# Kernel optimization log

Measured on AMD Instinct MI355X. Metric: run time of the kernel, lower is better.

The kernel has to match this reference:

```python
import jax, jax.numpy as jnp
import numpy as np

B, K, P, N, COEF_D = 32, 2, 256, 8192, 10  # batch, parts, kp-per-part, cloud points
BETA = 0.1
SEP_FACTOR = 8.0
W_CHF, W_COV, W_SURF, W_JOINT, W_REG, W_SEP = 1.0, 1.0, 5.0, 1.0, 0.01, 2.0
# separation-loss pair indices (static, same as torch buffers select1/select2)
SEL1 = np.tile(np.arange(P), P - 1)
SEL2 = np.concatenate([np.arange(j, j + P) % P for j in range(1, P)])


def _pdist(a, b):
    # a: (..., M, 3), b: (..., N, 3) -> (..., M, N) euclidean distances
    d2 = (jnp.sum(a * a, -1)[..., :, None] + jnp.sum(b * b, -1)[..., None, :]
          - 2.0 * jnp.einsum('...mc,...nc->...mn', a, b))
    return jnp.sqrt(jnp.maximum(d2, 1e-12))


def _smooth_l1(pred, target, beta=BETA):
    d = jnp.abs(pred - target)
    return jnp.where(d < beta, 0.5 * d * d / beta, d - 0.5 * beta)


def setup_inputs() -> dict:
    key = jax.random.key(0)
    ks = jax.random.split(key, 10)
    return {
        'coefs': jax.random.normal(ks[0], (B, K * P, COEF_D), jnp.float32),
        'part_pred_kps': jax.random.normal(ks[1], (B, K, P, 3), jnp.float32),
        'part_nodes': jax.random.normal(ks[2], (B, K, P, 3), jnp.float32),
        'cloud': jax.random.normal(ks[3], (B, N, 3), jnp.float32),
        'cloud_cls': jax.random.randint(ks[4], (B, N), 0, K, jnp.int64),
        'pred_joint_loc': jax.random.normal(ks[5], (B, K - 1, 3), jnp.float32),
        'pred_joint_axis': jax.random.normal(ks[6], (B, K - 1, 3), jnp.float32),
        'gt_joint_loc': jax.random.normal(ks[7], (B, K - 1, 3), jnp.float32),
        'gt_joint_axis': jax.random.normal(ks[8], (B, K - 1, 3), jnp.float32),
        'gt_part_scale': jax.random.uniform(ks[9], (B, K, 3), jnp.float32),
    }


def _forward(coefs, part_pred_kps, part_nodes, cloud,
             pred_joint_loc, pred_joint_axis, gt_joint_loc, gt_joint_axis,
             gt_part_scale, cloud_cls):
    # ---- part chamfer (brute) over all parts at once: (B,K,M,N) ----
    d_chf = _pdist(part_pred_kps, part_nodes)
    fwd = jnp.min(d_chf, axis=3).mean(axis=(0, 2))   # (K,)
    bwd = jnp.min(d_chf, axis=2).mean(axis=(0, 2))   # (K,)
    chf_loss = jnp.mean(fwd + bwd)

    # ---- coverage loss: masked per-part pc extremes vs node extremes ----
    mask = cloud_cls[:, None, :] == jnp.arange(K)[None, :, None]  # (B,K,N)
    big = jnp.float32(1e9)
    pc = cloud[:, None, :, :]                                      # (B,1,N,3)
    pc_max = jnp.max(jnp.where(mask[..., None], pc, -big), axis=2)  # (B,K,3)
    pc_min = jnp.min(jnp.where(mask[..., None], pc, big), axis=2)
    kp_max = jnp.max(part_nodes, axis=2)                            # (B,K,3)
    kp_min = jnp.min(part_nodes, axis=2)
    cov_loss = jnp.mean((_smooth_l1(kp_max, pc_max) + _smooth_l1(kp_min, pc_min)) * 0.5)

    # ---- separation loss ----
    a = part_nodes[:, :, SEL1, :]
    b = part_nodes[:, :, SEL2, :]
    dist_sep = jnp.linalg.norm(a - b, axis=-1)                      # (B,K,L)
    thr = (jnp.linalg.norm(gt_part_scale, axis=-1) / SEP_FACTOR)[:, :, None]
    sep_loss = jnp.mean(jnp.maximum(0.0, thr - dist_sep))

    # ---- surface loss: single-side chamfer nodes -> cloud ----
    nodes = part_nodes.reshape(B, K * P, 3)
    d_surf = _pdist(nodes, cloud)                                   # (B, K*P, N)
    surf_loss = jnp.min(d_surf, axis=2).mean()

    # ---- joint loss ----
    dot = jnp.sum(pred_joint_axis * gt_joint_axis, -1)
    na = jnp.linalg.norm(pred_joint_axis, axis=-1)
    nb = jnp.linalg.norm(gt_joint_axis, axis=-1)
    loss_axis = 1.0 - (dot / jnp.maximum(na * nb, 1e-8)).mean()
    ngt = gt_joint_axis / jnp.linalg.norm(gt_joint_axis, axis=-1, keepdims=True)
    p = gt_joint_loc
    q = gt_joint_loc + ngt
    r = pred_joint_loc
    x = p - q
    t = jnp.sum((r - q) * x, -1, keepdims=True) / jnp.sum(x * x, -1, keepdims=True)
    loss_loc = jnp.linalg.norm(t * (p - q) + (q - r), axis=-1).mean()
    joint_loss = loss_loc * 1.0 + loss_axis * 0.5  # revolute: loc_weight=1, axis_weight=0.5

    reg_loss = jnp.mean(coefs * coefs)

    return (chf_loss * W_CHF + cov_loss * W_COV + surf_loss * W_SURF
            + joint_loss * W_JOINT + reg_loss * W_REG + sep_loss * W_SEP)


def reference(coefs, part_pred_kps, part_nodes, cloud, cloud_cls,
              pred_joint_loc, pred_joint_axis, gt_joint_loc, gt_joint_axis,
              gt_part_scale):
    return _forward(coefs, part_pred_kps, part_nodes, cloud,
                    pred_joint_loc, pred_joint_axis, gt_joint_loc,
                    gt_joint_axis, gt_part_scale, cloud_cls)
```

## Files before the change

kernel.cpp:

```cpp
#include <hip/hip_runtime.h>
#include <math.h>

#define NB 32
#define KK 2
#define PP 256
#define NCLOUD 8192
#define NNODES 512
#define NCOEF 163840
#define SURF0 385
#define NCHUNK 16
#define NSURF (NB * NCHUNK)
#define NBLK (SURF0 + NSURF)

#define SL_SEP 0
#define SL_COV 256
#define SL_REG 320
#define SL_JNT 384
#define PCHF 512
#define PART0 131584

__device__ inline float waveSum(float v) {
#pragma unroll
  for (int o = 32; o > 0; o >>= 1) v += __shfl_down(v, o);
  return v;
}
__device__ inline float waveMax(float v) {
#pragma unroll
  for (int o = 32; o > 0; o >>= 1) v = fmaxf(v, __shfl_down(v, o));
  return v;
}
__device__ inline float waveMin(float v) {
#pragma unroll
  for (int o = 32; o > 0; o >>= 1) v = fminf(v, __shfl_down(v, o));
  return v;
}
__device__ inline float smooth_l1(float d) {
  d = fabsf(d);
  return d < 0.1f ? 5.0f * d * d : d - 0.05f;
}

__global__ __launch_bounds__(256) void mega_kernel(
    const float* __restrict__ coefs,
    const float* __restrict__ preds,
    const float* __restrict__ nodes,
    const float* __restrict__ cloud,
    const int* __restrict__ cls,
    const float* __restrict__ pjl, const float* __restrict__ pja,
    const float* __restrict__ gjl, const float* __restrict__ gja,
    const float* __restrict__ gps,
    float* __restrict__ ws, float* __restrict__ out) {
  const int bid = blockIdx.x;
  const int t = threadIdx.x;
  const int wave = t >> 6, lane = t & 63;
  __shared__ float4 sh4[512];
  __shared__ float shg[2048];
  __shared__ float red[12][4];

  if (bid < 256) {
    const int bk = bid >> 2;
    const int h = bid & 3;
    const float* pb = preds + (size_t)bk * PP * 3;
    const float* nbp = nodes + (size_t)bk * PP * 3;
    {
      float x = pb[3 * t], y = pb[3 * t + 1], z = pb[3 * t + 2];
      sh4[t] = make_float4(x, y, z, x * x + y * y + z * z);
      x = nbp[3 * t]; y = nbp[3 * t + 1]; z = nbp[3 * t + 2];
      sh4[256 + t] = make_float4(x, y, z, x * x + y * y + z * z);
    }
    __syncthreads();
    float4 ptv[4], ntv[4];
#pragma unroll
    for (int q = 0; q < 4; ++q) {
      ptv[q] = sh4[lane + q * 64];
      ntv[q] = sh4[256 + lane + q * 64];
    }
    const float s0 = gps[bk * 3 + 0], s1 = gps[bk * 3 + 1], s2 = gps[bk * 3 + 2];
    const float thr = sqrtf(s0 * s0 + s1 * s1 + s2 * s2) * 0.125f;
    float g1[4], g2[4], sep = 0.0f;
#pragma unroll
    for (int q = 0; q < 4; ++q) { g1[q] = 1e30f; g2[q] = 1e30f; }
    const int j0 = h * 64 + wave * 16;
#pragma unroll 4
    for (int jj = 0; jj < 16; ++jj) {
      const int j = j0 + jj;
      const float4 pj = sh4[j];
      const float4 nj = sh4[256 + j];
#pragma unroll
      for (int q = 0; q < 4; ++q) {
        float dot = fmaf(ptv[q].x, nj.x, fmaf(ptv[q].y, nj.y, ptv[q].z * nj.z));
        g1[q] = fminf(g1[q], fmaf(-2.0f, dot, nj.w));
        dot = fmaf(ntv[q].x, pj.x, fmaf(ntv[q].y, pj.y, ntv[q].z * pj.z));
        g2[q] = fminf(g2[q], fmaf(-2.0f, dot, pj.w));
        dot = fmaf(ntv[q].x, nj.x, fmaf(ntv[q].y, nj.y, ntv[q].z * nj.z));
        const float d2 = fmaf(-2.0f, dot, ntv[q].w + nj.w);
        const float d = sqrtf(fmaxf(d2, 0.0f));
        if (j != lane + q * 64) sep += fmaxf(thr - d, 0.0f);
      }
    }
#pragma unroll
    for (int q = 0; q < 4; ++q) {
      shg[wave * 256 + lane + q * 64] = ptv[q].w + g1[q];
      shg[1024 + wave * 256 + lane + q * 64] = ntv[q].w + g2[q];
    }
    __syncthreads();
    float* pc = ws + PCHF + (size_t)bid * 512;
    pc[t] = fminf(fminf(shg[t], shg[256 + t]),
                  fminf(shg[512 + t], shg[768 + t]));
    pc[256 + t] = fminf(fminf(shg[1024 + t], shg[1280 + t]),
                        fminf(shg[1536 + t], shg[1792 + t]));
    sep = waveSum(sep);
    if (lane == 0) red[0][wave] = sep;
    __syncthreads();
    if (t == 0)
      ws[SL_SEP + bid] = red[0][0] + red[0][1] + red[0][2] + red[0][3];

  } else if (bid < 320) {
    const int bk = bid - 256;
    const int b = bk >> 1;
    const int k = bk & 1;
    float pmax0 = -1e9f, pmax1 = -1e9f, pmax2 = -1e9f;
    float pmin0 = 1e9f, pmin1 = 1e9f, pmin2 = 1e9f;
    const float* cb = cloud + (size_t)b * NCLOUD * 3;
    const int* lb = cls + (size_t)b * NCLOUD;
    for (int i = t; i < NCLOUD; i += 256) {
      if (lb[i] == k) {
        const float x = cb[i * 3 + 0], y = cb[i * 3 + 1], z = cb[i * 3 + 2];
        pmax0 = fmaxf(pmax0, x); pmax1 = fmaxf(pmax1, y); pmax2 = fmaxf(pmax2, z);
        pmin0 = fminf(pmin0, x); pmin1 = fminf(pmin1, y); pmin2 = fminf(pmin2, z);
      }
    }
    const float* nb = nodes + (size_t)bk * PP * 3;
    const float kx = nb[t * 3 + 0], ky = nb[t * 3 + 1], kz = nb[t * 3 + 2];
    pmax0 = waveMax(pmax0); pmax1 = waveMax(pmax1); pmax2 = waveMax(pmax2);
    pmin0 = waveMin(pmin0); pmin1 = waveMin(pmin1); pmin2 = waveMin(pmin2);
    float kmax0 = waveMax(kx), kmax1 = waveMax(ky), kmax2 = waveMax(kz);
    float kmin0 = waveMin(kx), kmin1 = waveMin(ky), kmin2 = waveMin(kz);
    if (lane == 0) {
      red[0][wave] = pmax0; red[1][wave] = pmax1; red[2][wave] = pmax2;
      red[3][wave] = pmin0; red[4][wave] = pmin1; red[5][wave] = pmin2;
      red[6][wave] = kmax0; red[7][wave] = kmax1; red[8][wave] = kmax2;
      red[9][wave] = kmin0; red[10][wave] = kmin1; red[11][wave] = kmin2;
    }
    __syncthreads();
    if (t == 0) {
      float v[12];
#pragma unroll
      for (int q = 0; q < 12; ++q) {
        if (q < 3 || (q >= 6 && q < 9))
          v[q] = fmaxf(fmaxf(red[q][0], red[q][1]), fmaxf(red[q][2], red[q][3]));
        else
          v[q] = fminf(fminf(red[q][0], red[q][1]), fminf(red[q][2], red[q][3]));
      }
      float s = 0.0f;
#pragma unroll
      for (int c2 = 0; c2 < 3; ++c2)
        s += 0.5f * (smooth_l1(v[6 + c2] - v[0 + c2]) + smooth_l1(v[9 + c2] - v[3 + c2]));
      ws[SL_COV + bk] = s;
    }

  } else if (bid < 384) {
    const int r = bid - 320;
    const float4* c4 = (const float4*)coefs;
    float v = 0.0f;
    for (int i = r * 256 + t; i < NCOEF / 4; i += 64 * 256) {
      const float4 q = c4[i];
      v += q.x * q.x + q.y * q.y + q.z * q.z + q.w * q.w;
    }
    v = waveSum(v);
    if (lane == 0) red[0][wave] = v;
    __syncthreads();
    if (t == 0)
      ws[SL_REG + r] = red[0][0] + red[0][1] + red[0][2] + red[0][3];

  } else if (bid == 384) {
    float cosv = 0.0f, locv = 0.0f;
    if (t < NB) {
      const float axj = pja[t * 3 + 0], ayj = pja[t * 3 + 1], azj = pja[t * 3 + 2];
      const float gx = gja[t * 3 + 0], gy = gja[t * 3 + 1], gz = gja[t * 3 + 2];
      const float dot = axj * gx + ayj * gy + azj * gz;
      const float na = sqrtf(axj * axj + ayj * ayj + azj * azj);
      const float nbn = sqrtf(gx * gx + gy * gy + gz * gz);
      cosv = dot / fmaxf(na * nbn, 1e-8f);
      const float ux = gx / nbn, uy = gy / nbn, uz = gz / nbn;
      const float px = gjl[t * 3 + 0], py = gjl[t * 3 + 1], pz = gjl[t * 3 + 2];
      const float qx = px + ux, qy = py + uy, qz = pz + uz;
      const float rx = pjl[t * 3 + 0], ry = pjl[t * 3 + 1], rz = pjl[t * 3 + 2];
      const float xx = px - qx, xy = py - qy, xz = pz - qz;
      const float tnum = (rx - qx) * xx + (ry - qy) * xy + (rz - qz) * xz;
      const float tden = xx * xx + xy * xy + xz * xz;
      const float tv = tnum / tden;
      const float vx = tv * xx + (qx - rx);
      const float vy = tv * xy + (qy - ry);
      const float vz = tv * xz + (qz - rz);
      locv = sqrtf(vx * vx + vy * vy + vz * vz);
    }
    cosv = waveSum(cosv);
    locv = waveSum(locv);
    if (t == 0) {
      ws[SL_JNT + 0] = cosv;
      ws[SL_JNT + 1] = locv;
      out[0] = 0.0f;
    }

  } else {
    const int s = bid - SURF0;
    const int b = s >> 4;
    const int c = s & 15;
    const float* cb = cloud + ((size_t)b * NCLOUD + (size_t)c * 512) * 3;
#pragma unroll
    for (int g = 0; g < 2; ++g) {
      const int idx = g * 256 + t;
      const float qx = cb[3 * idx], qy = cb[3 * idx + 1], qz = cb[3 * idx + 2];
      sh4[idx] = make_float4(qx, qy, qz, 0.5f * (qx * qx + qy * qy + qz * qz));
    }
    __syncthreads();
    const float* nb = nodes + (size_t)b * NNODES * 3;
    float nxv[8], nyv[8], nzv[8], mg[8];
#pragma unroll
    for (int q = 0; q < 8; ++q) {
      const int n = lane + q * 64;
      nxv[q] = nb[3 * n]; nyv[q] = nb[3 * n + 1]; nzv[q] = nb[3 * n + 2];
      mg[q] = 1e30f;
    }
    const int p0 = wave * 128;
#pragma unroll 4
    for (int j = 0; j < 128; ++j) {
      const float4 q4 = sh4[p0 + j];
#pragma unroll
      for (int q = 0; q < 8; ++q)
        mg[q] = fminf(mg[q],
                      fmaf(-nxv[q], q4.x,
                           fmaf(-nyv[q], q4.y, fmaf(-nzv[q], q4.z, q4.w))));
    }
#pragma unroll
    for (int q = 0; q < 8; ++q)
      shg[wave * 512 + lane + q * 64] = mg[q];
    __syncthreads();
    float* pout = ws + PART0 + ((size_t)b * NCHUNK + c) * NNODES;
#pragma unroll
    for (int g = 0; g < 2; ++g) {
      const int node = g * 256 + t;
      pout[node] = fminf(fminf(shg[node], shg[512 + node]),
                         fminf(shg[1024 + node], shg[1536 + node]));
    }
  }
}

__global__ __launch_bounds__(256) void final1_kernel(
    const float* __restrict__ nodes, const float* __restrict__ ws,
    float* __restrict__ out) {
  const int b = blockIdx.x;
  const int t = threadIdx.x;
  const int wave = t >> 6, lane = t & 63;
  const float* partial = ws + PART0;
  const float* nb = nodes + (size_t)b * NNODES * 3;
  float ssum = 0.0f;
#pragma unroll
  for (int g = 0; g < 2; ++g) {
    const int node = g * 256 + t;
    float m = 1e30f;
#pragma unroll
    for (int c = 0; c < NCHUNK; ++c)
      m = fminf(m, partial[((size_t)b * NCHUNK + c) * NNODES + node]);
    const float x = nb[3 * node], y = nb[3 * node + 1], z = nb[3 * node + 2];
    const float nn = x * x + y * y + z * z;
    ssum += sqrtf(fmaxf(fmaf(2.0f, m, nn), 1e-12f));
  }
  float csum = 0.0f;
#pragma unroll
  for (int k = 0; k < KK; ++k) {
    const int bk = b * KK + k;
    const float* q0 = ws + PCHF + (size_t)(4 * bk + 0) * 512;
    const float* q1 = ws + PCHF + (size_t)(4 * bk + 1) * 512;
    const float* q2 = ws + PCHF + (size_t)(4 * bk + 2) * 512;
    const float* q3 = ws + PCHF + (size_t)(4 * bk + 3) * 512;
    const float fwd = fminf(fminf(q0[t], q1[t]), fminf(q2[t], q3[t]));
    const float bwd = fminf(fminf(q0[256 + t], q1[256 + t]),
                            fminf(q2[256 + t], q3[256 + t]));
    csum += sqrtf(fmaxf(fwd, 1e-12f)) + sqrtf(fmaxf(bwd, 1e-12f));
  }
  ssum = waveSum(ssum);
  csum = waveSum(csum);
  __shared__ float r[2][4];
  if (lane == 0) { r[0][wave] = ssum; r[1][wave] = csum; }
  __syncthreads();
  if (t == 0) {
    const float ssum_t = r[0][0] + r[0][1] + r[0][2] + r[0][3];
    const float csum_t = r[1][0] + r[1][1] + r[1][2] + r[1][3];
    float v = ssum_t * (5.0f / (float)(NB * NNODES)) +
              csum_t * (1.0f / (float)(KK * NB * PP));
    float sep8 = 0.0f;
#pragma unroll
    for (int q = 0; q < 8; ++q) sep8 += ws[SL_SEP + 8 * b + q];
    v += sep8 * (2.0f / (float)(NB * KK * PP * (PP - 1)));
    v += (ws[SL_COV + 2 * b] + ws[SL_COV + 2 * b + 1]) *
         (1.0f / (float)(NB * KK * 3));
    v += (ws[SL_REG + 2 * b] + ws[SL_REG + 2 * b + 1]) * (0.01f / (float)NCOEF);
    if (b == 0) {
      const float axis = 1.0f - ws[SL_JNT + 0] / (float)NB;
      const float loc = ws[SL_JNT + 1] / (float)NB;
      v += loc + 0.5f * axis;
    }
    atomicAdd(out, v);
  }
}

extern "C" void kernel_launch(void* const* d_in, const int* in_sizes, int n_in,
                              void* d_out, int out_size, void* d_ws, size_t ws_size,
                              hipStream_t stream) {
  const float* coefs = (const float*)d_in[0];
  const float* preds = (const float*)d_in[1];
  const float* nodes = (const float*)d_in[2];
  const float* cloud = (const float*)d_in[3];
  const int* cls = (const int*)d_in[4];
  const float* pjl = (const float*)d_in[5];
  const float* pja = (const float*)d_in[6];
  const float* gjl = (const float*)d_in[7];
  const float* gja = (const float*)d_in[8];
  const float* gps = (const float*)d_in[9];
  float* out = (float*)d_out;
  float* ws = (float*)d_ws;

  mega_kernel<<<NBLK, 256, 0, stream>>>(coefs, preds, nodes, cloud, cls,
                                        pjl, pja, gjl, gja, gps, ws, out);
  final1_kernel<<<NB, 256, 0, stream>>>(nodes, ws, out);
}
```

Measured before the change: 24.88 us.

## Reorder mega-kernel blocks, pack surface loop with float2 FMA, split final reduction

Surface-distance blocks, the heaviest work, now come first in the block index order so they are scheduled before the lighter chamfer, coverage and reg blocks. Their inner loop pairs two cloud points in an interleaved shared-memory layout so each step can use packed 2-wide FMA (v_pk_fma) on negated node coordinates. The final kernel uses two blocks per batch instead of one to spread the reduction across more CUs. This adds more atomics on the output and a denser LDS layout, and relies on the compiler actually emitting the packed instructions.

```diff
diff --git a/kernel.cpp b/kernel.cpp
--- a/kernel.cpp
+++ b/kernel.cpp
@@ -7,10 +7,13 @@
 #define NCLOUD 8192
 #define NNODES 512
 #define NCOEF 163840
-#define SURF0 385
 #define NCHUNK 16
 #define NSURF (NB * NCHUNK)
-#define NBLK (SURF0 + NSURF)
+#define CHAM0 512
+#define NBLK 897
+
+typedef float v2f __attribute__((ext_vector_type(2)));
+typedef float v4f __attribute__((ext_vector_type(4)));
 
 #define SL_SEP 0
 #define SL_COV 256
@@ -52,13 +55,65 @@
   const int bid = blockIdx.x;
   const int t = threadIdx.x;
   const int wave = t >> 6, lane = t & 63;
-  __shared__ float4 sh4[512];
-  __shared__ float shg[2048];
+  __shared__ float smem[4096];
   __shared__ float red[12][4];
 
-  if (bid < 256) {
-    const int bk = bid >> 2;
-    const int h = bid & 3;
+  if (bid < CHAM0) {
+    const int b = bid >> 4;
+    const int c = bid & 15;
+    const float* cb = cloud + ((size_t)b * NCLOUD + (size_t)c * 512) * 3;
+#pragma unroll
+    for (int g = 0; g < 2; ++g) {
+      const int p = g * 256 + t;
+      const float qx = cb[3 * p], qy = cb[3 * p + 1], qz = cb[3 * p + 2];
+      const float qh = 0.5f * (qx * qx + qy * qy + qz * qz);
+      float* base = &smem[(p >> 1) * 8 + (p & 1)];
+      base[0] = qx; base[2] = qy; base[4] = qz; base[6] = qh;
+    }
+    __syncthreads();
+    const float* nb = nodes + (size_t)b * NNODES * 3;
+    v2f nx2[8], ny2[8], nz2[8];
+    float mg[8];
+#pragma unroll
+    for (int q = 0; q < 8; ++q) {
+      const int n = lane + q * 64;
+      const float nx = nb[3 * n], ny = nb[3 * n + 1], nz = nb[3 * n + 2];
+      nx2[q] = (v2f){-nx, -nx}; ny2[q] = (v2f){-ny, -ny}; nz2[q] = (v2f){-nz, -nz};
+      mg[q] = 1e30f;
+    }
+    const int p0 = wave * 64;
+#pragma unroll 2
+    for (int i = 0; i < 64; ++i) {
+      const v4f A = *(const v4f*)&smem[(p0 + i) * 8];
+      const v4f Bv = *(const v4f*)&smem[(p0 + i) * 8 + 4];
+      const v2f X = A.xy, Y = A.zw, Z = Bv.xy, H = Bv.zw;
+#pragma unroll
+      for (int q = 0; q < 8; ++q) {
+        const v2f g = __builtin_elementwise_fma(
+            nx2[q], X,
+            __builtin_elementwise_fma(
+                ny2[q], Y, __builtin_elementwise_fma(nz2[q], Z, H)));
+        mg[q] = fminf(fminf(mg[q], g.x), g.y);
+      }
+    }
+    __syncthreads();
+#pragma unroll
+    for (int q = 0; q < 8; ++q) smem[wave * 512 + lane + q * 64] = mg[q];
+    __syncthreads();
+    float* pout = ws + PART0 + ((size_t)b * NCHUNK + c) * NNODES;
+#pragma unroll
+    for (int g = 0; g < 2; ++g) {
+      const int node = g * 256 + t;
+      pout[node] = fminf(fminf(smem[node], smem[512 + node]),
+                         fminf(smem[1024 + node], smem[1536 + node]));
+    }
+
+  } else if (bid < 768) {
+    const int u = bid - CHAM0;
+    const int bk = u >> 2;
+    const int h = u & 3;
+    float4* sh4 = (float4*)smem;
+    float* shg = smem + 2048;
     const float* pb = preds + (size_t)bk * PP * 3;
     const float* nbp = nodes + (size_t)bk * PP * 3;
     {
@@ -103,7 +158,7 @@
       shg[1024 + wave * 256 + lane + q * 64] = ntv[q].w + g2[q];
     }
     __syncthreads();
-    float* pc = ws + PCHF + (size_t)bid * 512;
+    float* pc = ws + PCHF + (size_t)u * 512;
     pc[t] = fminf(fminf(shg[t], shg[256 + t]),
                   fminf(shg[512 + t], shg[768 + t]));
     pc[256 + t] = fminf(fminf(shg[1024 + t], shg[1280 + t]),
@@ -112,10 +167,10 @@
     if (lane == 0) red[0][wave] = sep;
     __syncthreads();
     if (t == 0)
-      ws[SL_SEP + bid] = red[0][0] + red[0][1] + red[0][2] + red[0][3];
-
-  } else if (bid < 320) {
-    const int bk = bid - 256;
+      ws[SL_SEP + u] = red[0][0] + red[0][1] + red[0][2] + red[0][3];
+
+  } else if (bid < 832) {
+    const int bk = bid - 768;
     const int b = bk >> 1;
     const int k = bk & 1;
     float pmax0 = -1e9f, pmax1 = -1e9f, pmax2 = -1e9f;
@@ -158,8 +213,8 @@
       ws[SL_COV + bk] = s;
     }
 
-  } else if (bid < 384) {
-    const int r = bid - 320;
+  } else if (bid < 896) {
+    const int r = bid - 832;
     const float4* c4 = (const float4*)coefs;
     float v = 0.0f;
     for (int i = r * 256 + t; i < NCOEF / 4; i += 64 * 256) {
@@ -172,7 +227,7 @@
     if (t == 0)
       ws[SL_REG + r] = red[0][0] + red[0][1] + red[0][2] + red[0][3];
 
-  } else if (bid == 384) {
+  } else {
     float cosv = 0.0f, locv = 0.0f;
     if (t < NB) {
       const float axj = pja[t * 3 + 0], ayj = pja[t * 3 + 1], azj = pja[t * 3 + 2];
@@ -201,75 +256,29 @@
       ws[SL_JNT + 1] = locv;
       out[0] = 0.0f;
     }
-
-  } else {
-    const int s = bid - SURF0;
-    const int b = s >> 4;
-    const int c = s & 15;
-    const float* cb = cloud + ((size_t)b * NCLOUD + (size_t)c * 512) * 3;
-#pragma unroll
-    for (int g = 0; g < 2; ++g) {
-      const int idx = g * 256 + t;
-      const float qx = cb[3 * idx], qy = cb[3 * idx + 1], qz = cb[3 * idx + 2];
-      sh4[idx] = make_float4(qx, qy, qz, 0.5f * (qx * qx + qy * qy + qz * qz));
-    }
-    __syncthreads();
-    const float* nb = nodes + (size_t)b * NNODES * 3;
-    float nxv[8], nyv[8], nzv[8], mg[8];
-#pragma unroll
-    for (int q = 0; q < 8; ++q) {
-      const int n = lane + q * 64;
-      nxv[q] = nb[3 * n]; nyv[q] = nb[3 * n + 1]; nzv[q] = nb[3 * n + 2];
-      mg[q] = 1e30f;
-    }
-    const int p0 = wave * 128;
-#pragma unroll 4
-    for (int j = 0; j < 128; ++j) {
-      const float4 q4 = sh4[p0 + j];
-#pragma unroll
-      for (int q = 0; q < 8; ++q)
-        mg[q] = fminf(mg[q],
-                      fmaf(-nxv[q], q4.x,
-                           fmaf(-nyv[q], q4.y, fmaf(-nzv[q], q4.z, q4.w))));
-    }
-#pragma unroll
-    for (int q = 0; q < 8; ++q)
-      shg[wave * 512 + lane + q * 64] = mg[q];
-    __syncthreads();
-    float* pout = ws + PART0 + ((size_t)b * NCHUNK + c) * NNODES;
-#pragma unroll
-    for (int g = 0; g < 2; ++g) {
-      const int node = g * 256 + t;
-      pout[node] = fminf(fminf(shg[node], shg[512 + node]),
-                         fminf(shg[1024 + node], shg[1536 + node]));
-    }
   }
 }
 
 __global__ __launch_bounds__(256) void final1_kernel(
     const float* __restrict__ nodes, const float* __restrict__ ws,
     float* __restrict__ out) {
-  const int b = blockIdx.x;
+  const int b = blockIdx.x >> 1;
+  const int half = blockIdx.x & 1;
   const int t = threadIdx.x;
   const int wave = t >> 6, lane = t & 63;
   const float* partial = ws + PART0;
   const float* nb = nodes + (size_t)b * NNODES * 3;
-  float ssum = 0.0f;
-#pragma unroll
-  for (int g = 0; g < 2; ++g) {
-    const int node = g * 256 + t;
-    float m = 1e30f;
-#pragma unroll
-    for (int c = 0; c < NCHUNK; ++c)
-      m = fminf(m, partial[((size_t)b * NCHUNK + c) * NNODES + node]);
-    const float x = nb[3 * node], y = nb[3 * node + 1], z = nb[3 * node + 2];
-    const float nn = x * x + y * y + z * z;
-    ssum += sqrtf(fmaxf(fmaf(2.0f, m, nn), 1e-12f));
-  }
+  const int node = half * 256 + t;
+  float m = 1e30f;
+#pragma unroll
+  for (int c = 0; c < NCHUNK; ++c)
+    m = fminf(m, partial[((size_t)b * NCHUNK + c) * NNODES + node]);
+  const float x = nb[3 * node], y = nb[3 * node + 1], z = nb[3 * node + 2];
+  const float nn = x * x + y * y + z * z;
+  float ssum = sqrtf(fmaxf(fmaf(2.0f, m, nn), 1e-12f));
   float csum = 0.0f;
-#pragma unroll
-  for (int k = 0; k < KK; ++k) {
-    const int bk = b * KK + k;
+  {
+    const int bk = b * KK + half;
     const float* q0 = ws + PCHF + (size_t)(4 * bk + 0) * 512;
     const float* q1 = ws + PCHF + (size_t)(4 * bk + 1) * 512;
     const float* q2 = ws + PCHF + (size_t)(4 * bk + 2) * 512;
@@ -277,7 +286,7 @@
     const float fwd = fminf(fminf(q0[t], q1[t]), fminf(q2[t], q3[t]));
     const float bwd = fminf(fminf(q0[256 + t], q1[256 + t]),
                             fminf(q2[256 + t], q3[256 + t]));
-    csum += sqrtf(fmaxf(fwd, 1e-12f)) + sqrtf(fmaxf(bwd, 1e-12f));
+    csum = sqrtf(fmaxf(fwd, 1e-12f)) + sqrtf(fmaxf(bwd, 1e-12f));
   }
   ssum = waveSum(ssum);
   csum = waveSum(csum);
@@ -289,14 +298,13 @@
     const float csum_t = r[1][0] + r[1][1] + r[1][2] + r[1][3];
     float v = ssum_t * (5.0f / (float)(NB * NNODES)) +
               csum_t * (1.0f / (float)(KK * NB * PP));
-    float sep8 = 0.0f;
-#pragma unroll
-    for (int q = 0; q < 8; ++q) sep8 += ws[SL_SEP + 8 * b + q];
-    v += sep8 * (2.0f / (float)(NB * KK * PP * (PP - 1)));
-    v += (ws[SL_COV + 2 * b] + ws[SL_COV + 2 * b + 1]) *
-         (1.0f / (float)(NB * KK * 3));
-    v += (ws[SL_REG + 2 * b] + ws[SL_REG + 2 * b + 1]) * (0.01f / (float)NCOEF);
-    if (b == 0) {
+    float sep4 = 0.0f;
+#pragma unroll
+    for (int q = 0; q < 4; ++q) sep4 += ws[SL_SEP + 8 * b + 4 * half + q];
+    v += sep4 * (2.0f / (float)(NB * KK * PP * (PP - 1)));
+    v += ws[SL_COV + 2 * b + half] * (1.0f / (float)(NB * KK * 3));
+    v += ws[SL_REG + blockIdx.x] * (0.01f / (float)NCOEF);
+    if (blockIdx.x == 0) {
       const float axis = 1.0f - ws[SL_JNT + 0] / (float)NB;
       const float loc = ws[SL_JNT + 1] / (float)NB;
       v += loc + 0.5f * axis;
@@ -323,5 +331,5 @@
 
   mega_kernel<<<NBLK, 256, 0, stream>>>(coefs, preds, nodes, cloud, cls,
                                         pjl, pja, gjl, gja, gps, ws, out);
-  final1_kernel<<<NB, 256, 0, stream>>>(nodes, ws, out);
-}
+  final1_kernel<<<2 * NB, 256, 0, stream>>>(nodes, ws, out);
+}
```

New measurement: 27.97 us. +12.4%, slower.
